# Kernel tuning notes

Hardware: AMD Instinct MI355X
Metric: run time of the kernel (lower is better)

## Reference

```python
import jax, jax.numpy as jnp
import numpy as np

# Module constants (from init_kwargs / derived)
KH, KW = 3, 3
STRIDE = (1, 1)
PAD = (1, 1)
DIL = (1, 1)
N_OFFSET_GRPS = 8  # offset.shape[1] // (2*KH*KW) = 144 // 18
N_WEIGHT_GRPS = 1


def setup_inputs() -> dict:
    key = jax.random.key(0)
    k1, k2, k3, k4, k5 = jax.random.split(key, 5)
    B, C, H, W = 4, 64, 128, 128
    inp = {
        "input": jax.random.normal(k1, (B, C, H, W), dtype=jnp.float32),
        "offset": jax.random.normal(k2, (B, 2 * N_OFFSET_GRPS * KH * KW, H, W), dtype=jnp.float32),
        "mask": jax.random.uniform(k3, (B, N_OFFSET_GRPS * KH * KW, H, W), dtype=jnp.float32),
        "weight": jax.random.normal(k4, (64, C, KH, KW), dtype=jnp.float32) * 0.05,
        "bias": jax.random.normal(k5, (64,), dtype=jnp.float32) * 0.05,
    }
    return inp


def _deform_conv2d(x, offset, mask, weight, bias):
    B, C, H, W = x.shape
    Ho, Wo = offset.shape[2], offset.shape[3]
    G = N_OFFSET_GRPS
    K = KH * KW
    Cg = C // G

    # base (un-deformed) sampling positions per kernel tap and output pixel
    ky, kx = jnp.meshgrid(jnp.arange(KH), jnp.arange(KW), indexing="ij")
    ky = ky.reshape(K)
    kx = kx.reshape(K)
    oy = jnp.arange(Ho) * STRIDE[0] - PAD[0]
    ox = jnp.arange(Wo) * STRIDE[1] - PAD[1]
    base_y = (oy[None, :, None] + (ky * DIL[0])[:, None, None]).astype(x.dtype)  # [K,Ho,1]
    base_x = (ox[None, None, :] + (kx * DIL[1])[:, None, None]).astype(x.dtype)  # [K,1,Wo]

    off = offset.reshape(B, G, K, 2, Ho, Wo)  # [...,0]=dy, [...,1]=dx
    py = base_y[None, None] + off[:, :, :, 0]  # [B,G,K,Ho,Wo]
    px = base_x[None, None] + off[:, :, :, 1]

    y0 = jnp.floor(py)
    x0 = jnp.floor(px)
    ly = py - y0  # fractional parts
    lx = px - x0
    y0i = y0.astype(jnp.int32)
    x0i = x0.astype(jnp.int32)

    xg = x.reshape(B, G, Cg, H * W)  # per-offset-group channel slices

    def corner(yi, xi):
        valid = ((yi >= 0) & (yi < H) & (xi >= 0) & (xi < W)).astype(x.dtype)
        idx = jnp.clip(yi, 0, H - 1) * W + jnp.clip(xi, 0, W - 1)  # [B,G,K,Ho,Wo]
        gather = lambda xbg, ibg: xbg[:, ibg]  # [Cg,H*W],[K,Ho,Wo] -> [Cg,K,Ho,Wo]
        v = jax.vmap(jax.vmap(gather))(xg, idx)  # [B,G,Cg,K,Ho,Wo]
        return v * valid[:, :, None]

    w00 = (1 - ly) * (1 - lx)
    w01 = (1 - ly) * lx
    w10 = ly * (1 - lx)
    w11 = ly * lx
    samp = (corner(y0i, x0i) * w00[:, :, None]
            + corner(y0i, x0i + 1) * w01[:, :, None]
            + corner(y0i + 1, x0i) * w10[:, :, None]
            + corner(y0i + 1, x0i + 1) * w11[:, :, None])  # [B,G,Cg,K,Ho,Wo]

    samp = samp * mask.reshape(B, G, 1, K, Ho, Wo)  # DCNv2 modulation
    col = samp.reshape(B, C, K, Ho, Wo)
    wr = weight.reshape(weight.shape[0], C, K)  # groups == 1
    out = jnp.einsum("ock,bckhw->bohw", wr, col) + bias[None, :, None, None]
    return out


def reference(input, offset, mask, weight, bias):
    return _deform_conv2d(input, offset, mask, weight, bias)
```

## Files before the change

kernel.cpp:

```cpp
#include <hip/hip_runtime.h>

#define HH 128
#define WW 128
#define CC 64
#define CO 64
#define BB 4
#define GG 8
#define CG 8
#define KK 9
#define HW (HH*WW)
#define PXT 16
#define NCH 18
#define NPOS (GG*KK*PXT)

typedef __attribute__((ext_vector_type(8))) short short8;
typedef __attribute__((ext_vector_type(4))) float floatx4;
typedef __attribute__((ext_vector_type(2))) float f32x2;

union S8I { short8 s; int i[4]; };
union FU { float f; unsigned u; };

__device__ inline short f2bf(float f) {
    FU v; v.f = f;
    return (short)((v.u + 0x7FFF + ((v.u >> 16) & 1)) >> 16);
}
__device__ inline unsigned rnd2(float f) {
    FU v; v.f = f;
    return v.u + 0x8000u;
}
__device__ inline float bflo(int e) { union { int i; float f; } u; u.i = e << 16; return u.f; }
__device__ inline float bfhi(int e) { union { int i; float f; } u; u.i = e & 0xffff0000; return u.f; }

__global__ __launch_bounds__(256)
void prep(const float* __restrict__ wt, const float* __restrict__ in,
          short* __restrict__ wf, short* __restrict__ in_t) {
    const int bid = blockIdx.x;
    if (bid < 144) {
        const int tid = bid * 256 + threadIdx.x;
        const int j  = tid & 7;
        const int L  = (tid >> 3) & 63;
        const int fid = tid >> 9;
        const int ot = fid & 3;
        const int gc = fid >> 2;
        const int kpp = gc * 32 + (L >> 4) * 8 + j;
        const int o   = ot * 16 + (L & 15);
        const int cg  = kpp & 7;
        const int g   = (kpp >> 3) & 7;
        const int kk  = kpp >> 6;
        wf[tid] = f2bf(wt[o * 576 + (g * 8 + cg) * 9 + kk]);
    } else {
        const int idx = bid - 144;
        const int bx = idx & 63;
        const int g  = (idx >> 6) & 7;
        const int b  = idx >> 9;
        const int p  = bx * 256 + threadIdx.x;
        const float* src = in + (b * CC + g * CG) * HW + p;
        short8 v;
        #pragma unroll
        for (int cg = 0; cg < CG; ++cg) v[cg] = f2bf(src[cg * HW]);
        *(short8*)(in_t + ((b * GG + g) * HW + p) * 8) = v;
    }
}

__global__ __launch_bounds__(256)
void dcn_fused(const short* __restrict__ in_t, const float* __restrict__ off,
               const float* __restrict__ msk, const short* __restrict__ wf,
               const float* __restrict__ bias, float* __restrict__ out)
{
    __shared__ short s_col[NCH * 512];

    const int pxbase = blockIdx.x * PXT;
    const int ho = blockIdx.y;
    const int b  = blockIdx.z;
    const int t  = threadIdx.x;
    const int w = t >> 6, lane = t & 63;

    float pdy[5], pdx[5], pm[5];
    #pragma unroll
    for (int i = 0; i < 5; ++i) {
        const int pidx = t + i * 256;
        if (pidx < NPOS) {
            const int g  = (pidx >> 4) & 7;
            const int kk = pidx >> 7;
            const int base = ho * WW + pxbase + (pidx & 15);
            const int offc = (b * 144 + g * 18 + kk * 2) * HW + base;
            pdy[i] = off[offc];
            pdx[i] = off[offc + HW];
            pm[i]  = msk[(b * 72 + g * 9 + kk) * HW + base];
        }
    }

    const int q4 = lane >> 4, n16 = lane & 15;
    floatx4 acc0, acc1;
    #pragma unroll
    for (int r = 0; r < 4; ++r) { acc0[r] = bias[w * 16 + q4 * 4 + r]; acc1[r] = 0.f; }

    const short* inb = in_t + (long)b * GG * HW * 8;

    S8I u00[5], u01[5], u10[5], u11[5];
    float w00[5], w01[5], w10[5], w11[5];
    #pragma unroll
    for (int i = 0; i < 5; ++i) {
        const int pidx = t + i * 256;
        if (pidx < NPOS) {
            const int g  = (pidx >> 4) & 7;
            const int kk = pidx >> 7;
            const int px = pxbase + (pidx & 15);
            const int ky = kk / 3, kx = kk - ky * 3;

            const float py  = (float)(ho - 1 + ky) + pdy[i];
            const float pxf = (float)(px - 1 + kx) + pdx[i];
            const float y0f = floorf(py), x0f = floorf(pxf);
            const float ly = py - y0f, lx = pxf - x0f;
            const int y0 = (int)y0f, x0 = (int)x0f;
            const int y1 = y0 + 1,  x1 = x0 + 1;

            const float vy0 = (y0 >= 0 && y0 < HH) ? 1.f : 0.f;
            const float vy1 = (y1 >= 0 && y1 < HH) ? 1.f : 0.f;
            const float vx0 = (x0 >= 0 && x0 < WW) ? 1.f : 0.f;
            const float vx1 = (x1 >= 0 && x1 < WW) ? 1.f : 0.f;
            const int y0c = min(max(y0, 0), HH - 1), y1c = min(max(y1, 0), HH - 1);
            const int x0c = min(max(x0, 0), WW - 1), x1c = min(max(x1, 0), WW - 1);

            const float m = pm[i];
            const float wy0 = (1.f - ly) * vy0 * m;
            const float wy1 = ly * vy1 * m;
            const float wx0 = (1.f - lx) * vx0;
            const float wx1 = lx * vx1;
            w00[i] = wy0 * wx0;  w01[i] = wy0 * wx1;
            w10[i] = wy1 * wx0;  w11[i] = wy1 * wx1;

            const int gsh = g << 18;
            const int y0sh = gsh + (y0c << 11), y1sh = gsh + (y1c << 11);
            const int x0sh = x0c << 4, x1sh = x1c << 4;
            const char* ib = (const char*)inb;
            u00[i].s = *(const short8*)(ib + (y0sh + x0sh));
            u01[i].s = *(const short8*)(ib + (y0sh + x1sh));
            u10[i].s = *(const short8*)(ib + (y1sh + x0sh));
            u11[i].s = *(const short8*)(ib + (y1sh + x1sh));
        }
    }

    #pragma unroll
    for (int i = 0; i < 5; ++i) {
        const int pidx = t + i * 256;
        if (pidx < NPOS) {
            const f32x2 W00 = {w00[i], w00[i]}, W01 = {w01[i], w01[i]};
            const f32x2 W10 = {w10[i], w10[i]}, W11 = {w11[i], w11[i]};
            S8I res;
            #pragma unroll
            for (int pc = 0; pc < 4; ++pc) {
                const int e00 = u00[i].i[pc], e01 = u01[i].i[pc];
                const int e10 = u10[i].i[pc], e11 = u11[i].i[pc];
                f32x2 a00 = {bflo(e00), bfhi(e00)};
                f32x2 a01 = {bflo(e01), bfhi(e01)};
                f32x2 a10 = {bflo(e10), bfhi(e10)};
                f32x2 a11 = {bflo(e11), bfhi(e11)};
                f32x2 v = a00 * W00;
                v += a01 * W01;
                v += a10 * W10;
                v += a11 * W11;
                res.i[pc] = (int)__builtin_amdgcn_perm(rnd2(v.y), rnd2(v.x), 0x07060302u);
            }
            *(short8*)(s_col + pidx * 8) = res.s;
        }
    }

    __syncthreads();

    #pragma unroll
    for (int gc = 0; gc < NCH; ++gc) {
        const short8 bfr = *(const short8*)&s_col[(gc * 64 + lane) * 8];
        const short8 afr = *(const short8*)&wf[((gc * 4 + w) * 64 + lane) * 8];
        if (gc & 1) acc1 = __builtin_amdgcn_mfma_f32_16x16x32_bf16(afr, bfr, acc1, 0, 0, 0);
        else        acc0 = __builtin_amdgcn_mfma_f32_16x16x32_bf16(afr, bfr, acc0, 0, 0, 0);
    }

    const int px = pxbase + n16;
    #pragma unroll
    for (int r = 0; r < 4; ++r) {
        const int o = w * 16 + q4 * 4 + r;
        out[((b * CO + o) * HH + ho) * WW + px] = acc0[r] + acc1[r];
    }
}

extern "C" void kernel_launch(void* const* d_in, const int* in_sizes, int n_in,
                              void* d_out, int out_size, void* d_ws, size_t ws_size,
                              hipStream_t stream) {
    const float* in   = (const float*)d_in[0];
    const float* off  = (const float*)d_in[1];
    const float* msk  = (const float*)d_in[2];
    const float* wt   = (const float*)d_in[3];
    const float* bias = (const float*)d_in[4];
    float* out = (float*)d_out;
    short* wf   = (short*)d_ws;
    short* in_t = (short*)d_ws + 36864;

    prep<<<144 + 2048, 256, 0, stream>>>(wt, in, wf, in_t);

    dim3 grid(WW / PXT, HH, BB);
    dcn_fused<<<grid, 256, 0, stream>>>(in_t, off, msk, wf, bias, out);
}
```

Before: 143.6 us.

## Widen pixel tile to 64 and split channel groups into two MFMA phases

Each block now handles 64 output pixels instead of 16. Work is split into two halves of four offset groups, and each wave samples one group for all 9 taps across 64 lanes, so offset and mask loads are contiguous per lane. Every wave then computes all four output-channel tiles per pixel slice, and the weight fragment layout is re-permuted to match. This cuts block count and per-pixel overhead and gives more MFMA work per shared-memory fragment. The cost is a second barrier, more accumulator registers, and 4x fewer blocks.

```diff
diff --git a/kernel.cpp b/kernel.cpp
--- a/kernel.cpp
+++ b/kernel.cpp
@@ -9,9 +9,7 @@
 #define CG 8
 #define KK 9
 #define HW (HH*WW)
-#define PXT 16
-#define NCH 18
-#define NPOS (GG*KK*PXT)
+#define PXT 64
 
 typedef __attribute__((ext_vector_type(8))) short short8;
 typedef __attribute__((ext_vector_type(4))) float floatx4;
@@ -37,17 +35,15 @@
     const int bid = blockIdx.x;
     if (bid < 144) {
         const int tid = bid * 256 + threadIdx.x;
-        const int j  = tid & 7;
-        const int L  = (tid >> 3) & 63;
+        const int j   = tid & 7;
+        const int L   = (tid >> 3) & 63;
         const int fid = tid >> 9;
-        const int ot = fid & 3;
-        const int gc = fid >> 2;
-        const int kpp = gc * 32 + (L >> 4) * 8 + j;
+        const int ot  = fid & 3;
+        const int gch = fid >> 2;
+        const int h   = gch / 9, gc = gch - h * 9;
         const int o   = ot * 16 + (L & 15);
-        const int cg  = kpp & 7;
-        const int g   = (kpp >> 3) & 7;
-        const int kk  = kpp >> 6;
-        wf[tid] = f2bf(wt[o * 576 + (g * 8 + cg) * 9 + kk]);
+        const int g   = h * 4 + (L >> 4);
+        wf[tid] = f2bf(wt[o * 576 + (g * 8 + j) * 9 + gc]);
     } else {
         const int idx = bid - 144;
         const int bx = idx & 63;
@@ -62,51 +58,50 @@
     }
 }
 
-__global__ __launch_bounds__(256)
+__global__ __launch_bounds__(256, 4)
 void dcn_fused(const short* __restrict__ in_t, const float* __restrict__ off,
                const float* __restrict__ msk, const short* __restrict__ wf,
                const float* __restrict__ bias, float* __restrict__ out)
 {
-    __shared__ short s_col[NCH * 512];
+    __shared__ short s_col[9 * 4 * 512];
 
     const int pxbase = blockIdx.x * PXT;
     const int ho = blockIdx.y;
     const int b  = blockIdx.z;
     const int t  = threadIdx.x;
     const int w = t >> 6, lane = t & 63;
+    const int px = pxbase + lane;
+    const int q4 = lane >> 4, n16 = lane & 15;
+    const int basepix = ho * WW + px;
 
-    float pdy[5], pdx[5], pm[5];
+    floatx4 acc[4];
     #pragma unroll
-    for (int i = 0; i < 5; ++i) {
-        const int pidx = t + i * 256;
-        if (pidx < NPOS) {
-            const int g  = (pidx >> 4) & 7;
-            const int kk = pidx >> 7;
-            const int base = ho * WW + pxbase + (pidx & 15);
-            const int offc = (b * 144 + g * 18 + kk * 2) * HW + base;
+    for (int ot = 0; ot < 4; ++ot)
+        #pragma unroll
+        for (int r = 0; r < 4; ++r)
+            acc[ot][r] = bias[ot * 16 + q4 * 4 + r];
+
+    const char* ib = (const char*)(in_t + (long)b * GG * HW * 8);
+
+    #pragma unroll
+    for (int h = 0; h < 2; ++h) {
+        const int g = h * 4 + w;
+
+        float pdy[9], pdx[9], pm[9];
+        #pragma unroll
+        for (int i = 0; i < 9; ++i) {
+            const int offc = (b * 144 + g * 18 + i * 2) * HW + basepix;
             pdy[i] = off[offc];
             pdx[i] = off[offc + HW];
-            pm[i]  = msk[(b * 72 + g * 9 + kk) * HW + base];
+            pm[i]  = msk[(b * 72 + g * 9 + i) * HW + basepix];
         }
-    }
 
-    const int q4 = lane >> 4, n16 = lane & 15;
-    floatx4 acc0, acc1;
-    #pragma unroll
-    for (int r = 0; r < 4; ++r) { acc0[r] = bias[w * 16 + q4 * 4 + r]; acc1[r] = 0.f; }
+        if (h) __syncthreads();
 
-    const short* inb = in_t + (long)b * GG * HW * 8;
-
-    S8I u00[5], u01[5], u10[5], u11[5];
-    float w00[5], w01[5], w10[5], w11[5];
-    #pragma unroll
-    for (int i = 0; i < 5; ++i) {
-        const int pidx = t + i * 256;
-        if (pidx < NPOS) {
-            const int g  = (pidx >> 4) & 7;
-            const int kk = pidx >> 7;
-            const int px = pxbase + (pidx & 15);
-            const int ky = kk / 3, kx = kk - ky * 3;
+        const int gsh = g << 18;
+        #pragma unroll
+        for (int i = 0; i < 9; ++i) {
+            const int ky = i / 3, kx = i - (i / 3) * 3;
 
             const float py  = (float)(ho - 1 + ky) + pdy[i];
             const float pxf = (float)(px - 1 + kx) + pdx[i];
@@ -127,31 +122,24 @@
             const float wy1 = ly * vy1 * m;
             const float wx0 = (1.f - lx) * vx0;
             const float wx1 = lx * vx1;
-            w00[i] = wy0 * wx0;  w01[i] = wy0 * wx1;
-            w10[i] = wy1 * wx0;  w11[i] = wy1 * wx1;
+            const float w00 = wy0 * wx0, w01 = wy0 * wx1;
+            const float w10 = wy1 * wx0, w11 = wy1 * wx1;
 
-            const int gsh = g << 18;
             const int y0sh = gsh + (y0c << 11), y1sh = gsh + (y1c << 11);
             const int x0sh = x0c << 4, x1sh = x1c << 4;
-            const char* ib = (const char*)inb;
-            u00[i].s = *(const short8*)(ib + (y0sh + x0sh));
-            u01[i].s = *(const short8*)(ib + (y0sh + x1sh));
-            u10[i].s = *(const short8*)(ib + (y1sh + x0sh));
-            u11[i].s = *(const short8*)(ib + (y1sh + x1sh));
-        }
-    }
+            S8I u00, u01, u10, u11;
+            u00.s = *(const short8*)(ib + (y0sh + x0sh));
+            u01.s = *(const short8*)(ib + (y0sh + x1sh));
+            u10.s = *(const short8*)(ib + (y1sh + x0sh));
+            u11.s = *(const short8*)(ib + (y1sh + x1sh));
 
-    #pragma unroll
-    for (int i = 0; i < 5; ++i) {
-        const int pidx = t + i * 256;
-        if (pidx < NPOS) {
-            const f32x2 W00 = {w00[i], w00[i]}, W01 = {w01[i], w01[i]};
-            const f32x2 W10 = {w10[i], w10[i]}, W11 = {w11[i], w11[i]};
+            const f32x2 W00 = {w00, w00}, W01 = {w01, w01};
+            const f32x2 W10 = {w10, w10}, W11 = {w11, w11};
             S8I res;
             #pragma unroll
             for (int pc = 0; pc < 4; ++pc) {
-                const int e00 = u00[i].i[pc], e01 = u01[i].i[pc];
-                const int e10 = u10[i].i[pc], e11 = u11[i].i[pc];
+                const int e00 = u00.i[pc], e01 = u01.i[pc];
+                const int e10 = u10.i[pc], e11 = u11.i[pc];
                 f32x2 a00 = {bflo(e00), bfhi(e00)};
                 f32x2 a01 = {bflo(e01), bfhi(e01)};
                 f32x2 a10 = {bflo(e10), bfhi(e10)};
@@ -162,26 +150,29 @@
                 v += a11 * W11;
                 res.i[pc] = (int)__builtin_amdgcn_perm(rnd2(v.y), rnd2(v.x), 0x07060302u);
             }
-            *(short8*)(s_col + pidx * 8) = res.s;
+
+            *(short8*)(s_col + ((i * 4 + q4) * 64 + w * 16 + n16) * 8) = res.s;
+        }
+
+        __syncthreads();
+
+        #pragma unroll
+        for (int gc = 0; gc < 9; ++gc) {
+            const short8 bfr = *(const short8*)&s_col[((gc * 4 + w) * 64 + lane) * 8];
+            #pragma unroll
+            for (int ot = 0; ot < 4; ++ot) {
+                const short8 afr = *(const short8*)&wf[((h * 9 + gc) * 4 + ot) * 512 + lane * 8];
+                acc[ot] = __builtin_amdgcn_mfma_f32_16x16x32_bf16(afr, bfr, acc[ot], 0, 0, 0);
+            }
         }
     }
 
-    __syncthreads();
-
+    const int pxo = pxbase + w * 16 + n16;
     #pragma unroll
-    for (int gc = 0; gc < NCH; ++gc) {
-        const short8 bfr = *(const short8*)&s_col[(gc * 64 + lane) * 8];
-        const short8 afr = *(const short8*)&wf[((gc * 4 + w) * 64 + lane) * 8];
-        if (gc & 1) acc1 = __builtin_amdgcn_mfma_f32_16x16x32_bf16(afr, bfr, acc1, 0, 0, 0);
-        else        acc0 = __builtin_amdgcn_mfma_f32_16x16x32_bf16(afr, bfr, acc0, 0, 0, 0);
-    }
-
-    const int px = pxbase + n16;
-    #pragma unroll
-    for (int r = 0; r < 4; ++r) {
-        const int o = w * 16 + q4 * 4 + r;
-        out[((b * CO + o) * HH + ho) * WW + px] = acc0[r] + acc1[r];
-    }
+    for (int ot = 0; ot < 4; ++ot)
+        #pragma unroll
+        for (int r = 0; r < 4; ++r)
+            out[((b * CO + ot * 16 + q4 * 4 + r) * HH + ho) * WW + pxo] = acc[ot][r];
 }
 
 extern "C" void kernel_launch(void* const* d_in, const int* in_sizes, int n_in,
```

Result: faster. 136.8 us (-4.7%).
